# Performance work log

Hardware: AMD Instinct MI355X
Metric: run time of the kernel (lower is better)

The kernel has to match this reference:

```python
import jax, jax.numpy as jnp
import numpy as np

B, T, E, V, A = 8192, 64, 128, 32000, 10


def setup_inputs() -> dict:
    key = jax.random.key(0)
    ks = jax.random.split(key, 8)
    return {
        "utterance": jax.random.randint(ks[0], (B, T), 0, V + 1, dtype=jnp.int64)
            if jax.config.jax_enable_x64 else jax.random.randint(ks[0], (B, T), 0, V + 1).astype(jnp.int32),
        "global_idxes": jnp.arange(B, dtype=jnp.int32),
        "emb_table": jax.random.normal(ks[1], (V + 1, E), jnp.float32) * 0.1,
        "w_ih": jax.random.normal(ks[2], (3 * E, E), jnp.float32) * 0.1,
        "w_hh": jax.random.normal(ks[3], (3 * E, E), jnp.float32) * 0.1,
        "b_ih": jax.random.normal(ks[4], (3 * E,), jnp.float32) * 0.1,
        "b_hh": jax.random.normal(ks[5], (3 * E,), jnp.float32) * 0.1,
        "w_out": jax.random.normal(ks[6], (A, E), jnp.float32) * 0.1,
        "b_out": jax.random.normal(ks[7], (A,), jnp.float32) * 0.1,
    }


def _gru_cell(x, h, w_ih, w_hh, b_ih, b_hh):
    # PyTorch GRUCell math
    gi = x @ w_ih.T + b_ih  # [B, 3E]
    gh = h @ w_hh.T + b_hh  # [B, 3E]
    i_r, i_z, i_n = jnp.split(gi, 3, axis=-1)
    h_r, h_z, h_n = jnp.split(gh, 3, axis=-1)
    r = jax.nn.sigmoid(i_r + h_r)
    z = jax.nn.sigmoid(i_z + h_z)
    n = jnp.tanh(i_n + r * h_n)
    return (1.0 - z) * n + z * h


def reference(utterance, global_idxes, emb_table, w_ih, w_hh, b_ih, b_hh, w_out, b_out):
    bsz = utterance.shape[0]
    h0 = jnp.zeros((bsz, emb_table.shape[1]), emb_table.dtype)
    alive0 = jnp.ones((bsz,), jnp.bool_)

    def step(carry, tok):
        h, out, alive = carry
        emb = emb_table[tok]                      # [B, E] gather
        h = _gru_cell(emb, h, w_ih, w_hh, b_ih, b_hh)
        # output_state only written for rows still alive entering this step
        out = jnp.where(alive[:, None], h, out)
        alive = alive & (tok != 0)                # mark_dead AFTER writing state
        return (h, out, alive), None

    tokens = utterance.T                          # [T, B]
    (_, out_state, _), _ = jax.lax.scan(step, (h0, h0, alive0), tokens)
    logits = out_state @ w_out.T + b_out          # [B, A]
    action_probs = jax.nn.softmax(logits, axis=-1)
    return action_probs
```

## Files before the change

kernel.cpp:

```cpp
#include <hip/hip_runtime.h>
#include <hip/hip_fp16.h>

#define Tt 64
#define Ee 128
#define Aa 10
#define Vv 32001

typedef __attribute__((ext_vector_type(8))) _Float16 half8;
typedef __attribute__((ext_vector_type(4))) _Float16 half4;
typedef __attribute__((ext_vector_type(4))) float f32x4;

#define L2E 1.44269504f

__device__ __forceinline__ float fast_rcp(float x) { return __builtin_amdgcn_rcpf(x); }
__device__ __forceinline__ float fast_exp2(float x) {
#if __has_builtin(__builtin_amdgcn_exp2f)
    return __builtin_amdgcn_exp2f(x);
#else
    return __expf(x * 0.69314718056f);
#endif
}

__device__ __forceinline__ half8 load_h8(const float* p) {
    f32x4 a = *(const f32x4*)p;
    f32x4 b = *(const f32x4*)(p + 4);
    half8 r;
    r[0] = (_Float16)a[0]; r[1] = (_Float16)a[1]; r[2] = (_Float16)a[2]; r[3] = (_Float16)a[3];
    r[4] = (_Float16)b[0]; r[5] = (_Float16)b[1]; r[6] = (_Float16)b[2]; r[7] = (_Float16)b[3];
    return r;
}
__device__ __forceinline__ half8 load_h8s(const float* p, float s) {
    f32x4 a = *(const f32x4*)p;
    f32x4 b = *(const f32x4*)(p + 4);
    half8 r;
#pragma unroll
    for (int j = 0; j < 4; ++j) { r[j] = (_Float16)(a[j] * s); r[4 + j] = (_Float16)(b[j] * s); }
    return r;
}

#define MFMA_F16(a, b, c)  __builtin_amdgcn_mfma_f32_16x16x32_f16(a, b, c, 0, 0, 0)

__global__ __launch_bounds__(512, 2) void gi_precompute(
    const float* __restrict__ emb, const float* __restrict__ w_ih,
    const float* __restrict__ b_ih, const float* __restrict__ b_hh,
    char* __restrict__ gw) {
    __shared__ __align__(16) char xs[8192];
    const int tid = threadIdx.x;
    const int wv = tid >> 6;
    const int ln = tid & 63;
    const int fn = ln & 15;
    const int kg = ln >> 4;
    const int v0 = blockIdx.x * 32;
    const int gc = wv * 16 + fn;
    const int srow = tid >> 4;
    const int c8 = (tid & 15) << 3;

    {
        int v = v0 + srow; if (v >= Vv) v = Vv - 1;
        half8 hx = load_h8(emb + (size_t)v * Ee + c8);
        int off = (srow * 256 + c8 * 2) ^ ((srow & 7) << 4);
        *(half8*)(xs + off) = hx;
    }
    half8 wr[4], wz[4], wn[4];
#pragma unroll
    for (int kt = 0; kt < 4; ++kt) {
        int k0 = kt * 32 + kg * 8;
        wr[kt] = load_h8(w_ih + (size_t)gc * Ee + k0);
        wz[kt] = load_h8(w_ih + (size_t)(128 + gc) * Ee + k0);
        wn[kt] = load_h8(w_ih + (size_t)(256 + gc) * Ee + k0);
    }
    const float bcr = b_ih[gc] + b_hh[gc];
    const float bcz = b_ih[128 + gc] + b_hh[128 + gc];
    const float bcn = b_ih[256 + gc];
    __syncthreads();

    f32x4 ar[2], az[2], an[2];
#pragma unroll
    for (int mt = 0; mt < 2; ++mt) {
        ar[mt] = (f32x4){0.f, 0.f, 0.f, 0.f};
        az[mt] = (f32x4){0.f, 0.f, 0.f, 0.f};
        an[mt] = (f32x4){0.f, 0.f, 0.f, 0.f};
    }
#pragma unroll
    for (int kt = 0; kt < 4; ++kt)
#pragma unroll
        for (int mt = 0; mt < 2; ++mt) {
            int r = mt * 16 + fn;
            int off = (r * 256 + (kt * 32 + kg * 8) * 2) ^ ((r & 7) << 4);
            half8 ha = *(const half8*)(xs + off);
            ar[mt] = MFMA_F16(ha, wr[kt], ar[mt]);
            az[mt] = MFMA_F16(ha, wz[kt], az[mt]);
            an[mt] = MFMA_F16(ha, wn[kt], an[mt]);
        }
#pragma unroll
    for (int mt = 0; mt < 2; ++mt)
#pragma unroll
        for (int i = 0; i < 4; ++i) {
            int v = v0 + mt * 16 + kg * 4 + i;
            if (v < Vv) {
                half4 g;
                g[0] = (_Float16)((ar[mt][i] + bcr) * (-L2E));
                g[1] = (_Float16)((az[mt][i] + bcz) * (-L2E));
                g[2] = (_Float16)((an[mt][i] + bcn) * (2.f * L2E));
                g[3] = (_Float16)0.f;
                *(half4*)(gw + (size_t)v * 1024 + gc * 8) = g;
            }
        }
}

#define SM_BYTES 26240

struct GateState {
    f32x4 h, o;
    int ts[4];
    half4 g[4];
};

template <bool WR>
__device__ __forceinline__ void gates_step(
    const f32x4& ar, const f32x4& az, const f32x4& an,
    GateState& st, int s, float bhn2, char* wbase, const int* wof) {
#pragma unroll
    for (int i = 0; i < 4; ++i) {
        float prp = ar[i] + (float)st.g[i][0];
        float pzp = az[i] + (float)st.g[i][1];
        float ea = fast_exp2(prp);
        float eb = fast_exp2(pzp);
        float da = 1.f + ea, db = 1.f + eb;
        float R = fast_rcp(da * db);
        float rr = db * R;
        float zz = da * R;
        float pnp = (float)st.g[i][2] + rr * (an[i] + bhn2);
        float ec = fast_exp2(pnp);
        float nn = 1.f - 2.f * fast_rcp(ec + 1.f);
        float h = nn + zz * (st.h[i] - nn);
        st.h[i] = h;
        if (s == st.ts[i]) st.o[i] = h;
        if (WR) *(_Float16*)(wbase + wof[i]) = (_Float16)h;
    }
}

__global__ __launch_bounds__(512, 1) void gru_dual_kernel(
    const int* __restrict__ utt, const char* __restrict__ gwc,
    const float* __restrict__ w_hh, const float* __restrict__ b_hh,
    const float* __restrict__ w_out, const float* __restrict__ b_out,
    float* __restrict__ out) {
    __shared__ __align__(16) char smem[SM_BYTES];
    int* tokb = (int*)smem;
    float* lg = (float*)(smem + 24576);
    int* tstar = (int*)(smem + 26112);
    float* outst = (float*)(smem + 8192);

    const int tid = threadIdx.x;
    const int wv = tid >> 6;
    const int ln = tid & 63;
    const int fn = ln & 15;
    const int kg = ln >> 4;
    const int row0 = blockIdx.x * 32;
    const int gc = wv * 16 + fn;
    const int gc8 = gc * 8;

    if (tid < 32) tstar[tid] = Tt - 1;
    *(float2*)(smem + 12288 + tid * 8) = (float2){0.f, 0.f};
    *(float2*)(smem + 20480 + tid * 8) = (float2){0.f, 0.f};
    __syncthreads();
    {
        int4 tv = ((const int4*)(utt + (size_t)row0 * Tt))[tid];
        int4 sv = {tv.x << 10, tv.y << 10, tv.z << 10, tv.w << 10};
        ((int4*)tokb)[tid] = sv;
        int row = tid >> 4;
        int tq = (tid & 15) << 2;
        if (tv.x == 0) atomicMin(&tstar[row], tq);
        if (tv.y == 0) atomicMin(&tstar[row], tq + 1);
        if (tv.z == 0) atomicMin(&tstar[row], tq + 2);
        if (tv.w == 0) atomicMin(&tstar[row], tq + 3);
    }
    half8 whr[4], whz[4], whn[4];
#pragma unroll
    for (int kt = 0; kt < 4; ++kt) {
        int k0 = kt * 32 + kg * 8;
        whr[kt] = load_h8s(w_hh + (size_t)gc * Ee + k0, -L2E);
        whz[kt] = load_h8s(w_hh + (size_t)(128 + gc) * Ee + k0, -L2E);
        whn[kt] = load_h8s(w_hh + (size_t)(256 + gc) * Ee + k0, 2.f * L2E);
    }
    const float bhn2 = b_hh[256 + gc] * (2.f * L2E);
    __syncthreads();

    int offk[4], wof[4];
#pragma unroll
    for (int kt = 0; kt < 4; ++kt)
        offk[kt] = (fn * 256 + (kt * 32 + kg * 8) * 2) ^ ((fn & 7) << 4);
#pragma unroll
    for (int i = 0; i < 4; ++i) {
        int row = kg * 4 + i;
        wof[i] = (row * 256 + gc * 2) ^ ((row & 7) << 4);
    }

    GateState A, B;
#pragma unroll
    for (int i = 0; i < 4; ++i) {
        A.h[i] = 0.f; A.o[i] = 0.f; B.h[i] = 0.f; B.o[i] = 0.f;
        A.ts[i] = tstar[kg * 4 + i];
        B.ts[i] = tstar[16 + kg * 4 + i];
        A.g[i] = *(const half4*)(gwc + (tokb[(kg * 4 + i) * 64] + gc8));
        B.g[i] = *(const half4*)(gwc + (tokb[(16 + kg * 4 + i) * 64] + gc8));
    }

    f32x4 arB = (f32x4){0.f, 0.f, 0.f, 0.f};
    f32x4 azB = arB, anB = arB;
    int aRd = 12288, aWr = 8192, bRW = 20480;

#pragma unroll 1
    for (int k = 0; k < Tt; ++k) {
        half8 fA[4];
#pragma unroll
        for (int kt = 0; kt < 4; ++kt)
            fA[kt] = *(const half8*)(smem + (aRd + offk[kt]));
        half4 gnxB[4];
#pragma unroll
        for (int i = 0; i < 4; ++i)
            gnxB[i] = *(const half4*)(gwc + (tokb[(16 + kg * 4 + i) * 64 + k] + gc8));
        if (k > 0)
            gates_step<true>(arB, azB, anB, B, k - 1, bhn2, smem + bRW, wof);
        f32x4 arA = (f32x4){0.f, 0.f, 0.f, 0.f};
        f32x4 azA = arA, anA = arA;
        __builtin_amdgcn_s_setprio(1);
#pragma unroll
        for (int kt = 0; kt < 4; ++kt) {
            arA = MFMA_F16(fA[kt], whr[kt], arA);
            azA = MFMA_F16(fA[kt], whz[kt], azA);
            anA = MFMA_F16(fA[kt], whn[kt], anA);
        }
        __builtin_amdgcn_s_setprio(0);
        __syncthreads();
        half8 fB[4];
#pragma unroll
        for (int kt = 0; kt < 4; ++kt)
            fB[kt] = *(const half8*)(smem + (bRW + offk[kt]));
        half4 gnxA[4];
        int t2 = (k < Tt - 1) ? k + 1 : Tt - 1;
#pragma unroll
        for (int i = 0; i < 4; ++i)
            gnxA[i] = *(const half4*)(gwc + (tokb[(kg * 4 + i) * 64 + t2] + gc8));
        gates_step<true>(arA, azA, anA, A, k, bhn2, smem + aWr, wof);
        arB = (f32x4){0.f, 0.f, 0.f, 0.f};
        azB = arB; anB = arB;
        __builtin_amdgcn_s_setprio(1);
#pragma unroll
        for (int kt = 0; kt < 4; ++kt) {
            arB = MFMA_F16(fB[kt], whr[kt], arB);
            azB = MFMA_F16(fB[kt], whz[kt], azB);
            anB = MFMA_F16(fB[kt], whn[kt], anB);
        }
        __builtin_amdgcn_s_setprio(0);
        __syncthreads();
#pragma unroll
        for (int i = 0; i < 4; ++i) { A.g[i] = gnxA[i]; B.g[i] = gnxB[i]; }
        aRd ^= 4096; aWr ^= 4096; bRW ^= 4096;
    }
    gates_step<false>(arB, azB, anB, B, Tt - 1, bhn2, nullptr, wof);

#pragma unroll
    for (int i = 0; i < 4; ++i) {
        outst[(kg * 4 + i) * Ee + gc] = A.o[i];
        outst[(16 + kg * 4 + i) * Ee + gc] = B.o[i];
    }
    __syncthreads();

    if (tid < 32 * Aa) {
        int r = tid / Aa, a = tid % Aa;
        const float* wo = w_out + a * Ee;
        const float* os = outst + r * Ee;
        float s = b_out[a];
#pragma unroll
        for (int j = 0; j < Ee; j += 4) {
            f32x4 o = *(const f32x4*)(os + j);
            f32x4 w4 = *(const f32x4*)(wo + j);
            s += o[0] * w4[0] + o[1] * w4[1] + o[2] * w4[2] + o[3] * w4[3];
        }
        lg[r * 12 + a] = s;
    }
    __syncthreads();
    if (tid < 32) {
        float v[Aa];
        float mx = -1e30f;
#pragma unroll
        for (int a = 0; a < Aa; ++a) {
            v[a] = lg[tid * 12 + a];
            mx = fmaxf(mx, v[a]);
        }
        float sum = 0.f;
#pragma unroll
        for (int a = 0; a < Aa; ++a) {
            v[a] = __expf(v[a] - mx);
            sum += v[a];
        }
        float inv = fast_rcp(sum);
#pragma unroll
        for (int a = 0; a < Aa; ++a) out[(size_t)(row0 + tid) * Aa + a] = v[a] * inv;
    }
}

#define FSM_BYTES 21312
__global__ __launch_bounds__(512, 2) void gru_fallback_kernel(
    const int* __restrict__ utt, const float* __restrict__ emb,
    const float* __restrict__ w_ih, const float* __restrict__ w_hh,
    const float* __restrict__ b_ih, const float* __restrict__ b_hh,
    const float* __restrict__ w_out, const float* __restrict__ b_out,
    float* __restrict__ out) {
    __shared__ __align__(16) char smem[FSM_BYTES];
    int* tokb = (int*)smem;
    float* lg = (float*)(smem + 20480);
    int* tstar = (int*)(smem + 21248);
    float* outst = (float*)(smem + 4096);

    const int tid = threadIdx.x;
    const int wv = tid >> 6;
    const int ln = tid & 63;
    const int fn = ln & 15;
    const int kg = ln >> 4;
    const int row0 = blockIdx.x * 16;
    const int gc = wv * 16 + fn;
    const int srow = tid >> 5;
    const int c4 = (tid & 31) << 2;

    if (tid < 16) tstar[tid] = Tt - 1;
    *(float2*)(smem + 12288 + tid * 8) = (float2){0.f, 0.f};
    __syncthreads();
    {
        int2 tv = ((const int2*)(utt + (size_t)row0 * Tt))[tid];
        ((int2*)tokb)[tid] = tv;
        int row = tid >> 5;
        int tq = (tid & 31) << 1;
        if (tv.x == 0) atomicMin(&tstar[row], tq);
        if (tv.y == 0) atomicMin(&tstar[row], tq + 1);
    }
    half8 wir[4], wiz[4], win[4], whr[4], whz[4], whn[4];
#pragma unroll
    for (int kt = 0; kt < 4; ++kt) {
        int k0 = kt * 32 + kg * 8;
        wir[kt] = load_h8(w_ih + (size_t)gc * Ee + k0);
        wiz[kt] = load_h8(w_ih + (size_t)(128 + gc) * Ee + k0);
        win[kt] = load_h8(w_ih + (size_t)(256 + gc) * Ee + k0);
        whr[kt] = load_h8(w_hh + (size_t)gc * Ee + k0);
        whz[kt] = load_h8(w_hh + (size_t)(128 + gc) * Ee + k0);
        whn[kt] = load_h8(w_hh + (size_t)(256 + gc) * Ee + k0);
    }
    const float bcr = b_ih[gc] + b_hh[gc];
    const float bcz = b_ih[128 + gc] + b_hh[128 + gc];
    const float bin = b_ih[256 + gc];
    const float bhn = b_hh[256 + gc];
    __syncthreads();
    int ts[4];
#pragma unroll
    for (int i = 0; i < 4; ++i) ts[i] = tstar[kg * 4 + i];
    {
        int tok = tokb[srow * Tt];
        f32x4 a = *(const f32x4*)(emb + (size_t)tok * Ee + c4);
        half4 hx;
#pragma unroll
        for (int j = 0; j < 4; ++j) hx[j] = (_Float16)a[j];
        int off = (srow * 256 + c4 * 2) ^ ((srow & 7) << 4);
        *(half4*)(smem + 4096 + off) = hx;
    }
    __syncthreads();
    f32x4 hreg = (f32x4){0.f, 0.f, 0.f, 0.f};
    f32x4 oreg = (f32x4){0.f, 0.f, 0.f, 0.f};
    int cur = 0;
#pragma unroll 1
    for (int t = 0; t < Tt; ++t) {
        f32x4 pa;
        if (t < Tt - 1) {
            int tok = tokb[srow * Tt + t + 1];
            pa = *(const f32x4*)(emb + (size_t)tok * Ee + c4);
        }
        const char* xb = smem + 4096 + cur * 4096;
        const char* hb = smem + 12288 + cur * 4096;
        f32x4 ar = (f32x4){0.f, 0.f, 0.f, 0.f};
        f32x4 az = (f32x4){0.f, 0.f, 0.f, 0.f};
        f32x4 ain = (f32x4){0.f, 0.f, 0.f, 0.f};
        f32x4 ahn = (f32x4){0.f, 0.f, 0.f, 0.f};
        __builtin_amdgcn_s_setprio(1);
#pragma unroll
        for (int kt = 0; kt < 4; ++kt) {
            int off = (fn * 256 + (kt * 32 + kg * 8) * 2) ^ ((fn & 7) << 4);
            half8 xa = *(const half8*)(xb + off);
            half8 ha = *(const half8*)(hb + off);
            ar = MFMA_F16(xa, wir[kt], ar);
            ar = MFMA_F16(ha, whr[kt], ar);
            az = MFMA_F16(xa, wiz[kt], az);
            az = MFMA_F16(ha, whz[kt], az);
            ain = MFMA_F16(xa, win[kt], ain);
            ahn = MFMA_F16(ha, whn[kt], ahn);
        }
        __builtin_amdgcn_s_setprio(0);
        char* hn = smem + 12288 + (cur ^ 1) * 4096;
#pragma unroll
        for (int i = 0; i < 4; ++i) {
            float pr = ar[i] + bcr;
            float pz = az[i] + bcz;
            float rr = fast_rcp(1.f + __expf(-pr));
            float zz = fast_rcp(1.f + __expf(-pz));
            float pn = ain[i] + bin + rr * (ahn[i] + bhn);
            float e2 = __expf(2.f * pn);
            float nn = 1.f - 2.f * fast_rcp(e2 + 1.f);
            float h = (1.f - zz) * nn + zz * hreg[i];
            hreg[i] = h;
            if (t == ts[i]) oreg[i] = h;
            if (t < Tt - 1) {
                int row = kg * 4 + i;
                int off = (row * 256 + gc * 2) ^ ((row & 7) << 4);
                *(_Float16*)(hn + off) = (_Float16)h;
            }
        }
        if (t < Tt - 1) {
            half4 hx;
#pragma unroll
            for (int j = 0; j < 4; ++j) hx[j] = (_Float16)pa[j];
            int off = (srow * 256 + c4 * 2) ^ ((srow & 7) << 4);
            *(half4*)(smem + 4096 + (cur ^ 1) * 4096 + off) = hx;
        }
        __syncthreads();
        cur ^= 1;
    }
#pragma unroll
    for (int i = 0; i < 4; ++i) outst[(kg * 4 + i) * Ee + gc] = oreg[i];
    __syncthreads();
    if (tid < 16 * Aa) {
        int r = tid / Aa, a = tid % Aa;
        const float* wo = w_out + a * Ee;
        const float* os = outst + r * Ee;
        float s = b_out[a];
#pragma unroll
        for (int j = 0; j < Ee; j += 4) {
            f32x4 o = *(const f32x4*)(os + j);
            f32x4 w4 = *(const f32x4*)(wo + j);
            s += o[0] * w4[0] + o[1] * w4[1] + o[2] * w4[2] + o[3] * w4[3];
        }
        lg[r * 12 + a] = s;
    }
    __syncthreads();
    if (tid < 16) {
        float v[Aa];
        float mx = -1e30f;
#pragma unroll
        for (int a = 0; a < Aa; ++a) {
            v[a] = lg[tid * 12 + a];
            mx = fmaxf(mx, v[a]);
        }
        float sum = 0.f;
#pragma unroll
        for (int a = 0; a < Aa; ++a) {
            v[a] = __expf(v[a] - mx);
            sum += v[a];
        }
        float inv = fast_rcp(sum);
#pragma unroll
        for (int a = 0; a < Aa; ++a) out[(size_t)(row0 + tid) * Aa + a] = v[a] * inv;
    }
}

extern "C" void kernel_launch(void* const* d_in, const int* in_sizes, int n_in,
                              void* d_out, int out_size, void* d_ws, size_t ws_size,
                              hipStream_t stream) {
    (void)in_sizes; (void)n_in; (void)out_size;
    const int* utt = (const int*)d_in[0];
    const float* emb = (const float*)d_in[2];
    const float* wih = (const float*)d_in[3];
    const float* whh = (const float*)d_in[4];
    const float* bih = (const float*)d_in[5];
    const float* bhh = (const float*)d_in[6];
    const float* wout = (const float*)d_in[7];
    const float* bout = (const float*)d_in[8];
    const size_t need = (size_t)Vv * 1024;
    if (ws_size >= need) {
        char* gw = (char*)d_ws;
        gi_precompute<<<dim3((Vv + 31) / 32), 512, 0, stream>>>(emb, wih, bih, bhh, gw);
        gru_dual_kernel<<<256, 512, 0, stream>>>(utt, gw, whh, bhh, wout, bout, (float*)d_out);
    } else {
        gru_fallback_kernel<<<512, 512, 0, stream>>>(utt, emb, wih, whh, bih, bhh, wout, bout,
                                                     (float*)d_out);
    }
}
```

Measured before the change: 133.1 us.

## Merge staggered A/B GRU halves into one step with a single barrier

Replaces the staggered schedule with a plain one. Before, the B group's gate math overlapped the A group's MFMAs, with two barriers per timestep. Now each timestep issues all MFMAs for both row groups, then runs both gate passes, then waits at one raw s_barrier behind an lgkmcnt wait. The input-gate preactivations and the hidden bias are loaded into the MFMA accumulators as initial values, removing per-element adds from the gate math. This halves the barriers per step, but gives up the overlap between gate math and matrix work, and the double-buffer addresses are now computed from k parity.

```diff
diff --git a/kernel.cpp b/kernel.cpp
--- a/kernel.cpp
+++ b/kernel.cpp
@@ -116,27 +116,24 @@
     half4 g[4];
 };
 
-template <bool WR>
-__device__ __forceinline__ void gates_step(
+__device__ __forceinline__ void gates_one(
     const f32x4& ar, const f32x4& az, const f32x4& an,
-    GateState& st, int s, float bhn2, char* wbase, const int* wof) {
+    GateState& st, int s, char* wbase, const int* wof, bool wr) {
 #pragma unroll
     for (int i = 0; i < 4; ++i) {
-        float prp = ar[i] + (float)st.g[i][0];
-        float pzp = az[i] + (float)st.g[i][1];
-        float ea = fast_exp2(prp);
-        float eb = fast_exp2(pzp);
+        float ea = fast_exp2(ar[i]);
+        float eb = fast_exp2(az[i]);
         float da = 1.f + ea, db = 1.f + eb;
         float R = fast_rcp(da * db);
         float rr = db * R;
         float zz = da * R;
-        float pnp = (float)st.g[i][2] + rr * (an[i] + bhn2);
+        float pnp = (float)st.g[i][2] + rr * an[i];
         float ec = fast_exp2(pnp);
         float nn = 1.f - 2.f * fast_rcp(ec + 1.f);
         float h = nn + zz * (st.h[i] - nn);
         st.h[i] = h;
         if (s == st.ts[i]) st.o[i] = h;
-        if (WR) *(_Float16*)(wbase + wof[i]) = (_Float16)h;
+        if (wr) *(_Float16*)(wbase + wof[i]) = (_Float16)h;
     }
 }
 
@@ -161,8 +158,8 @@
     const int gc8 = gc * 8;
 
     if (tid < 32) tstar[tid] = Tt - 1;
-    *(float2*)(smem + 12288 + tid * 8) = (float2){0.f, 0.f};
-    *(float2*)(smem + 20480 + tid * 8) = (float2){0.f, 0.f};
+    *(float2*)(smem + 8192 + tid * 8) = (float2){0.f, 0.f};
+    *(float2*)(smem + 16384 + tid * 8) = (float2){0.f, 0.f};
     __syncthreads();
     {
         int4 tv = ((const int4*)(utt + (size_t)row0 * Tt))[tid];
@@ -206,24 +203,28 @@
         B.g[i] = *(const half4*)(gwc + (tokb[(16 + kg * 4 + i) * 64] + gc8));
     }
 
-    f32x4 arB = (f32x4){0.f, 0.f, 0.f, 0.f};
-    f32x4 azB = arB, anB = arB;
-    int aRd = 12288, aWr = 8192, bRW = 20480;
-
 #pragma unroll 1
     for (int k = 0; k < Tt; ++k) {
-        half8 fA[4];
-#pragma unroll
-        for (int kt = 0; kt < 4; ++kt)
-            fA[kt] = *(const half8*)(smem + (aRd + offk[kt]));
-        half4 gnxB[4];
-#pragma unroll
-        for (int i = 0; i < 4; ++i)
-            gnxB[i] = *(const half4*)(gwc + (tokb[(16 + kg * 4 + i) * 64 + k] + gc8));
-        if (k > 0)
-            gates_step<true>(arB, azB, anB, B, k - 1, bhn2, smem + bRW, wof);
-        f32x4 arA = (f32x4){0.f, 0.f, 0.f, 0.f};
-        f32x4 azA = arA, anA = arA;
+        const char* hA = smem + 8192 + (k & 1) * 4096;
+        const char* hB = smem + 16384 + (k & 1) * 4096;
+        half8 fA[4], fB[4];
+#pragma unroll
+        for (int kt = 0; kt < 4; ++kt) fA[kt] = *(const half8*)(hA + offk[kt]);
+#pragma unroll
+        for (int kt = 0; kt < 4; ++kt) fB[kt] = *(const half8*)(hB + offk[kt]);
+        int t2 = (k < Tt - 1) ? k + 1 : Tt - 1;
+        half4 gnxA[4], gnxB[4];
+#pragma unroll
+        for (int i = 0; i < 4; ++i) {
+            gnxA[i] = *(const half4*)(gwc + (tokb[(kg * 4 + i) * 64 + t2] + gc8));
+            gnxB[i] = *(const half4*)(gwc + (tokb[(16 + kg * 4 + i) * 64 + t2] + gc8));
+        }
+        f32x4 arA, azA, anA, arB, azB, anB;
+#pragma unroll
+        for (int i = 0; i < 4; ++i) {
+            arA[i] = (float)A.g[i][0]; azA[i] = (float)A.g[i][1]; anA[i] = bhn2;
+            arB[i] = (float)B.g[i][0]; azB[i] = (float)B.g[i][1]; anB[i] = bhn2;
+        }
         __builtin_amdgcn_s_setprio(1);
 #pragma unroll
         for (int kt = 0; kt < 4; ++kt) {
@@ -231,21 +232,6 @@
             azA = MFMA_F16(fA[kt], whz[kt], azA);
             anA = MFMA_F16(fA[kt], whn[kt], anA);
         }
-        __builtin_amdgcn_s_setprio(0);
-        __syncthreads();
-        half8 fB[4];
-#pragma unroll
-        for (int kt = 0; kt < 4; ++kt)
-            fB[kt] = *(const half8*)(smem + (bRW + offk[kt]));
-        half4 gnxA[4];
-        int t2 = (k < Tt - 1) ? k + 1 : Tt - 1;
-#pragma unroll
-        for (int i = 0; i < 4; ++i)
-            gnxA[i] = *(const half4*)(gwc + (tokb[(kg * 4 + i) * 64 + t2] + gc8));
-        gates_step<true>(arA, azA, anA, A, k, bhn2, smem + aWr, wof);
-        arB = (f32x4){0.f, 0.f, 0.f, 0.f};
-        azB = arB; anB = arB;
-        __builtin_amdgcn_s_setprio(1);
 #pragma unroll
         for (int kt = 0; kt < 4; ++kt) {
             arB = MFMA_F16(fB[kt], whr[kt], arB);
@@ -253,13 +239,23 @@
             anB = MFMA_F16(fB[kt], whn[kt], anB);
         }
         __builtin_amdgcn_s_setprio(0);
-        __syncthreads();
+
+        char* wA = smem + 8192 + ((k + 1) & 1) * 4096;
+        char* wB = smem + 16384 + ((k + 1) & 1) * 4096;
+        bool wr = (k < Tt - 1);
+        gates_one(arA, azA, anA, A, k, wA, wof, wr);
+        gates_one(arB, azB, anB, B, k, wB, wof, wr);
 #pragma unroll
         for (int i = 0; i < 4; ++i) { A.g[i] = gnxA[i]; B.g[i] = gnxB[i]; }
-        aRd ^= 4096; aWr ^= 4096; bRW ^= 4096;
-    }
-    gates_step<false>(arB, azB, anB, B, Tt - 1, bhn2, nullptr, wof);
-
+        if (k < Tt - 1) {
+            __builtin_amdgcn_sched_barrier(0);
+            asm volatile("s_waitcnt lgkmcnt(0)" ::: "memory");
+            __builtin_amdgcn_s_barrier();
+            __builtin_amdgcn_sched_barrier(0);
+        }
+    }
+
+    __syncthreads();
 #pragma unroll
     for (int i = 0; i < 4; ++i) {
         outst[(kg * 4 + i) * Ee + gc] = A.o[i];
```

Measured after the change: 147.3 us. +10.6%, slower.
